# Kernel optimization log

Measured on AMD Instinct MI355X. Metric: run time of the kernel, lower is better.

Reference implementation:

```python
import jax, jax.numpy as jnp
import numpy as np

HIDDEN = 2048
N_HEADS = 16
N_KV_HEADS = 4
HEAD_DIM = HIDDEN // N_HEADS  # 128
BATCH = 1
SEQ = 2048
EPS = 1e-6


def _rms_norm(x, scale, eps=EPS):
    var = jnp.mean(jnp.square(x), axis=-1, keepdims=True)
    return x * jax.lax.rsqrt(var + eps) * scale


def _rotate_half(x):
    x1, x2 = jnp.split(x, 2, axis=-1)
    return jnp.concatenate((-x2, x1), axis=-1)


def setup_inputs() -> dict:
    key = jax.random.key(0)
    ks = jax.random.split(key, 8)
    hidden_states = jax.random.normal(ks[0], (BATCH, SEQ, HIDDEN), dtype=jnp.float32)
    # causal mask, broadcastable over [B, H, S, S]
    attention_mask = jnp.tril(jnp.ones((SEQ, SEQ), dtype=bool))[None, None, :, :]
    # standard RoPE tables, broadcastable against [B, S, H, D]
    inv_freq = 1.0 / (10000.0 ** (np.arange(0, HEAD_DIM, 2, dtype=np.float32) / HEAD_DIM))
    t = np.arange(SEQ, dtype=np.float32)
    freqs = np.outer(t, inv_freq)                      # [S, D/2]
    emb = np.concatenate([freqs, freqs], axis=-1)      # [S, D]
    cos = jnp.asarray(np.cos(emb))[:, None, :]         # [S, 1, D]
    sin = jnp.asarray(np.sin(emb))[:, None, :]
    s = 1.0 / np.sqrt(HIDDEN)
    Wq = jax.random.normal(ks[1], (HIDDEN, N_HEADS * HEAD_DIM), dtype=jnp.float32) * s
    Wk = jax.random.normal(ks[2], (HIDDEN, N_KV_HEADS * HEAD_DIM), dtype=jnp.float32) * s
    Wv = jax.random.normal(ks[3], (HIDDEN, N_KV_HEADS * HEAD_DIM), dtype=jnp.float32) * s
    Wo = jax.random.normal(ks[4], (HIDDEN, HIDDEN), dtype=jnp.float32) * s
    q_norm_scale = jnp.ones((HEAD_DIM,), dtype=jnp.float32)
    k_norm_scale = jnp.ones((HEAD_DIM,), dtype=jnp.float32)
    last_norm_scale = jnp.ones((HIDDEN,), dtype=jnp.float32)
    return {
        "hidden_states": hidden_states,
        "cos": cos,
        "sin": sin,
        "Wq": Wq,
        "Wk": Wk,
        "Wv": Wv,
        "Wo": Wo,
        "q_norm_scale": q_norm_scale,
        "k_norm_scale": k_norm_scale,
        "last_norm_scale": last_norm_scale,
        "attention_mask": attention_mask,
    }


def reference(hidden_states, cos, sin, Wq, Wk, Wv, Wo,
              q_norm_scale, k_norm_scale, last_norm_scale, attention_mask):
    B, S, _ = hidden_states.shape
    q = (hidden_states @ Wq).reshape(B, S, N_HEADS, HEAD_DIM)
    k = (hidden_states @ Wk).reshape(B, S, N_KV_HEADS, HEAD_DIM)
    v = (hidden_states @ Wv).reshape(B, S, N_KV_HEADS, HEAD_DIM)
    # per-head RMSNorm on Q/K
    q = _rms_norm(q, q_norm_scale)
    k = _rms_norm(k, k_norm_scale)
    # RoPE (cos/sin broadcast [S,1,D] -> [B,S,H,D])
    q = q * cos + _rotate_half(q) * sin
    k = k * cos + _rotate_half(k) * sin
    # GQA expansion
    groups = N_HEADS // N_KV_HEADS
    if groups > 1:
        k = jnp.repeat(k, groups, axis=2)
        v = jnp.repeat(v, groups, axis=2)
    out = jax.nn.dot_product_attention(q, k, v, mask=attention_mask)  # [B,S,H,D]
    out = out.reshape(B, S, HIDDEN) @ Wo
    return _rms_norm(out, last_norm_scale)
```

## Files before the change

### kernel.cpp

```cpp
#include <hip/hip_runtime.h>

typedef unsigned short u16;
typedef unsigned int u32;

#define S 2048
#define HID 2048
#define NH 16
#define NKV 4
#define D 128
#define QKVP 3072
#define QSCALE (0.08838834764831845f * 1.4426950408889634f)
#define NEG_INF -3.0e38f

typedef __attribute__((ext_vector_type(8))) short short8;
typedef __attribute__((ext_vector_type(4))) float f32x4;

__device__ __forceinline__ float bf2f(u16 u) {
  union { u32 i; float f; } c; c.i = ((u32)u) << 16; return c.f;
}
__device__ __forceinline__ u16 f2bf(float f) {
  union { float f; u32 i; } c; c.f = f;
  u32 x = c.i;
  u32 r = x + 0x7fffu + ((x >> 16) & 1u);
  return (u16)(r >> 16);
}

#if __has_builtin(__builtin_amdgcn_exp2f)
__device__ __forceinline__ float exp2_hw(float x) { return __builtin_amdgcn_exp2f(x); }
#else
__device__ __forceinline__ float exp2_hw(float x) { return exp2f(x); }
#endif

__device__ __forceinline__ u32 cvt_pk_bf16(float a, float b) {
  u32 r;
  asm("v_cvt_pk_bf16_f32 %0, %1, %2" : "=v"(r) : "v"(a), "v"(b));
  return r;
}

__device__ __forceinline__ void gload16(const u16* g, u16* l) {
  __builtin_amdgcn_global_load_lds(
      (const __attribute__((address_space(1))) u32*)g,
      (__attribute__((address_space(3))) u32*)l, 16, 0, 0);
}

__device__ __forceinline__ void transpose_body(const float* __restrict__ src,
                                               u16* __restrict__ dst,
                                               int N, int K, int nt, int kt,
                                               int t) {
  __shared__ float T[64][65];
#pragma unroll
  for (int it = 0; it < 4; ++it) {
    int r = it * 16 + (t >> 4), c = (t & 15) * 4;
    float4 v = *(const float4*)(src + (size_t)(kt + r) * N + nt + c);
    T[r][c] = v.x; T[r][c + 1] = v.y; T[r][c + 2] = v.z; T[r][c + 3] = v.w;
  }
  __syncthreads();
#pragma unroll
  for (int it = 0; it < 2; ++it) {
    int n = it * 32 + (t >> 3), k8 = (t & 7) * 8;
    ushort4 w0, w1;
    w0.x = f2bf(T[k8 + 0][n]); w0.y = f2bf(T[k8 + 1][n]);
    w0.z = f2bf(T[k8 + 2][n]); w0.w = f2bf(T[k8 + 3][n]);
    w1.x = f2bf(T[k8 + 4][n]); w1.y = f2bf(T[k8 + 5][n]);
    w1.z = f2bf(T[k8 + 6][n]); w1.w = f2bf(T[k8 + 7][n]);
    *(ushort4*)(dst + (size_t)(nt + n) * K + kt + k8) = w0;
    *(ushort4*)(dst + (size_t)(nt + n) * K + kt + k8 + 4) = w1;
  }
}

__global__ __launch_bounds__(256) void k_pre(const float* __restrict__ hidden,
                                             u16* __restrict__ Hb,
                                             const float* __restrict__ Wq,
                                             const float* __restrict__ Wk,
                                             const float* __restrict__ Wv,
                                             u16* __restrict__ WT) {
  const int bx = blockIdx.x, t = threadIdx.x;
  if (bx < 2048) {
    int i = (bx * 256 + t) * 8;
    float4 v0 = *(const float4*)(hidden + i);
    float4 v1 = *(const float4*)(hidden + i + 4);
    ushort4 w0, w1;
    w0.x = f2bf(v0.x); w0.y = f2bf(v0.y); w0.z = f2bf(v0.z); w0.w = f2bf(v0.w);
    w1.x = f2bf(v1.x); w1.y = f2bf(v1.y); w1.z = f2bf(v1.z); w1.w = f2bf(v1.w);
    *(ushort4*)(Hb + i) = w0;
    *(ushort4*)(Hb + i + 4) = w1;
    return;
  }
  const int id = bx - 2048;
  const int x = id % 48, y = id / 48;
  const float* src; u16* dst; int N, nt;
  if (x < 32)      { src = Wq; dst = WT;                    N = 2048; nt = x * 64; }
  else if (x < 40) { src = Wk; dst = WT + 2048ull * 2048;   N = 512;  nt = (x - 32) * 64; }
  else             { src = Wv; dst = WT + 2560ull * 2048;   N = 512;  nt = (x - 40) * 64; }
  transpose_body(src, dst, N, 2048, nt, y * 64, t);
}

__global__ __launch_bounds__(256) void k_transpose(const float* __restrict__ src,
                                                   u16* __restrict__ dst,
                                                   int N, int K) {
  transpose_body(src, dst, N, K, blockIdx.x * 64, blockIdx.y * 64, threadIdx.x);
}

__global__ __launch_bounds__(256) void k_vt(const u16* __restrict__ QKV,
                                            u16* __restrict__ Vt) {
  __shared__ u16 T[64][66];
  const int t = threadIdx.x;
  const int s0 = blockIdx.x * 64, d0 = blockIdx.y * 64;
#pragma unroll
  for (int it = 0; it < 4; ++it) {
    int r = it * 16 + (t >> 4), c = (t & 15) * 4;
    ushort4 v = *(const ushort4*)(QKV + (size_t)(s0 + r) * QKVP + 2560 + d0 + c);
    T[r][c] = v.x; T[r][c + 1] = v.y; T[r][c + 2] = v.z; T[r][c + 3] = v.w;
  }
  __syncthreads();
#pragma unroll
  for (int it = 0; it < 4; ++it) {
    int dd = it * 16 + (t >> 4), sc = (t & 15) * 4;
    ushort4 w;
    w.x = T[sc + 0][dd]; w.y = T[sc + 1][dd];
    w.z = T[sc + 2][dd]; w.w = T[sc + 3][dd];
    *(ushort4*)(Vt + (size_t)(d0 + dd) * S + s0 + sc) = w;
  }
}

__global__ __launch_bounds__(256) void k_gemm_mfma(const u16* __restrict__ A,
                                                   const u16* __restrict__ BT,
                                                   void* __restrict__ Cout,
                                                   int N, int K, int out_bf16) {
  __shared__ __align__(16) u16 As[2][64 * 64];
  __shared__ __align__(16) u16 Bs[2][128 * 64];
  const int t = threadIdx.x, w = t >> 6, lane = t & 63;
  const int l15 = lane & 15, quad = lane >> 4;
  const int m0 = blockIdx.y * 64, n0 = blockIdx.x * 128;

  const int srow = lane >> 3;
  const int schunk = (lane & 7) ^ srow;
  const u16* Agb = A + (size_t)(m0 + w * 8 + srow) * K + schunk * 8;
  const u16* Bgb = BT + (size_t)(n0 + w * 8 + srow) * K + schunk * 8;

  f32x4 acc[4][2];
#pragma unroll
  for (int i = 0; i < 4; ++i)
#pragma unroll
    for (int j = 0; j < 2; ++j) acc[i][j] = (f32x4){0.f, 0.f, 0.f, 0.f};

  auto STAGE = [&](int k0, int b) {
#pragma unroll
    for (int it = 0; it < 2; ++it)
      gload16(Agb + (size_t)it * 32 * K + k0, &As[b][(w * 8 + it * 32) * 64]);
#pragma unroll
    for (int it = 0; it < 4; ++it)
      gload16(Bgb + (size_t)it * 32 * K + k0, &Bs[b][(w * 8 + it * 32) * 64]);
  };

  STAGE(0, 0);
  __syncthreads();
  int cur = 0;
  for (int k0 = 0; k0 < K; k0 += 64) {
    if (k0 + 64 < K) STAGE(k0 + 64, cur ^ 1);

    short8 af[4][2], bf[2][2];
#pragma unroll
    for (int k2 = 0; k2 < 2; ++k2) {
      int ch = (k2 * 4 + quad) ^ (l15 & 7);
#pragma unroll
      for (int i = 0; i < 4; ++i)
        af[i][k2] = *(const short8*)&As[cur][(i * 16 + l15) * 64 + ch * 8];
#pragma unroll
      for (int j = 0; j < 2; ++j)
        bf[j][k2] = *(const short8*)&Bs[cur][(w * 32 + j * 16 + l15) * 64 + ch * 8];
    }
#pragma unroll
    for (int k2 = 0; k2 < 2; ++k2)
#pragma unroll
      for (int i = 0; i < 4; ++i)
#pragma unroll
        for (int j = 0; j < 2; ++j)
          acc[i][j] = __builtin_amdgcn_mfma_f32_16x16x32_bf16(af[i][k2], bf[j][k2], acc[i][j], 0, 0, 0);

    __syncthreads();
    cur ^= 1;
  }

  if (out_bf16) {
    u16* C = (u16*)Cout;
#pragma unroll
    for (int i = 0; i < 4; ++i)
#pragma unroll
      for (int j = 0; j < 2; ++j) {
        int col = n0 + w * 32 + j * 16 + l15;
#pragma unroll
        for (int r = 0; r < 4; ++r)
          C[(size_t)(m0 + i * 16 + quad * 4 + r) * N + col] = f2bf(acc[i][j][r]);
      }
  } else {
    float* C = (float*)Cout;
#pragma unroll
    for (int i = 0; i < 4; ++i)
#pragma unroll
      for (int j = 0; j < 2; ++j) {
        int col = n0 + w * 32 + j * 16 + l15;
#pragma unroll
        for (int r = 0; r < 4; ++r)
          C[(size_t)(m0 + i * 16 + quad * 4 + r) * N + col] = acc[i][j][r];
      }
  }
}

__global__ __launch_bounds__(256) void k_norm_rope(u16* __restrict__ QKV,
                                                   const float* __restrict__ qsc,
                                                   const float* __restrict__ ksc,
                                                   const float* __restrict__ cosp,
                                                   const float* __restrict__ sinp) {
  const int s = blockIdx.x;
  const int w = threadIdx.x >> 6, lane = threadIdx.x & 63;
  const int hh = blockIdx.y * 4 + w;
  u16* row; const float* sc; float scale;
  if (hh < NH) { row = QKV + (size_t)s * QKVP + hh * D;               sc = qsc; scale = QSCALE; }
  else         { row = QKV + (size_t)s * QKVP + 2048 + (hh - NH) * D; sc = ksc; scale = 1.0f; }
  const int d0 = lane * 2;
  u32 pr = *(const u32*)(row + d0);
  float x0 = bf2f((u16)(pr & 0xffffu)), x1 = bf2f((u16)(pr >> 16));
  float v = x0 * x0 + x1 * x1;
#pragma unroll
  for (int o = 32; o; o >>= 1) v += __shfl_xor(v, o, 64);
  float rinv = rsqrtf(v * (1.0f / 128.0f) + 1e-6f) * scale;
  float xn0 = x0 * rinv * sc[d0], xn1 = x1 * rinv * sc[d0 + 1];
  float p0 = __shfl_xor(xn0, 32, 64);
  float p1 = __shfl_xor(xn1, 32, 64);
  float sgn = (lane < 32) ? -1.f : 1.f;
  float2 c  = *(const float2*)(cosp + (size_t)s * D + d0);
  float2 sn = *(const float2*)(sinp + (size_t)s * D + d0);
  float o0 = xn0 * c.x + sgn * p0 * sn.x;
  float o1 = xn1 * c.y + sgn * p1 * sn.y;
  *(u32*)(row + d0) = cvt_pk_bf16(o0, o1);
}

#define KP 128
#define PTP 72

__global__ __launch_bounds__(256) void k_flash(const u16* __restrict__ QKV,
                                               const u16* __restrict__ Vt,
                                               u16* __restrict__ O) {
  const int h = blockIdx.y, g = h >> 2;
  const int qt = (h < 8) ? (31 - (int)blockIdx.x) : (int)blockIdx.x;
  const int t = threadIdx.x;
  const int w = t >> 6, lane = t & 63, l15 = lane & 15, quad = lane >> 4;

  __shared__ __align__(16) u16 Klds[2][64 * KP];
  __shared__ __align__(16) u16 Vlds[128 * 64];
  __shared__ __align__(16) u16 Pt[4][16 * PTP];

  const int qbase = qt * 64 + w * 16;
  const int qrow = qbase + l15;

  short8 qf[4];
  {
    const u16* qp = QKV + (size_t)qrow * QKVP + h * D + quad * 8;
#pragma unroll
    for (int c = 0; c < 4; ++c) qf[c] = *(const short8*)(qp + c * 32);
  }

  float m = NEG_INF, l = 0.f;
  f32x4 oacc[8];
#pragma unroll
  for (int nc = 0; nc < 8; ++nc) oacc[nc] = (f32x4){0.f, 0.f, 0.f, 0.f};

  const int nt = qt + 1;
  const int dd = t >> 3, cc = t & 7;

  auto KLOAD = [&](int j0, int b) {
#pragma unroll
    for (int it = 0; it < 4; ++it) {
      int rl = w * 16 + it * 4 + quad;
      int gchunk = (lane & 15) ^ (rl & 7);
      const u16* gp = QKV + (size_t)(j0 + rl) * QKVP + 2048 + g * D + gchunk * 8;
      gload16(gp, &Klds[b][(w * 16 + it * 4) * KP]);
    }
  };
  auto VLOAD = [&](int j0, uint4* vr) {
#pragma unroll
    for (int it = 0; it < 4; ++it)
      vr[it] = *(const uint4*)(Vt + (size_t)(g * D + dd + it * 32) * S + j0 + cc * 8);
  };
  auto VWRITE = [&](uint4* vr) {
#pragma unroll
    for (int it = 0; it < 4; ++it) {
      int d = dd + it * 32;
      *(uint4*)&Vlds[d * 64 + ((cc ^ (d & 7)) * 8)] = vr[it];
    }
  };
  auto QKT = [&](int b, f32x4* sa) {
#pragma unroll
    for (int sub = 0; sub < 4; ++sub) {
      f32x4 acc = {0.f, 0.f, 0.f, 0.f};
#pragma unroll
      for (int c = 0; c < 4; ++c) {
        int ch = (c * 4 + quad) ^ (l15 & 7);
        short8 kf = *(const short8*)&Klds[b][(sub * 16 + l15) * KP + ch * 8];
        acc = __builtin_amdgcn_mfma_f32_16x16x32_bf16(kf, qf[c], acc, 0, 0, 0);
      }
      sa[sub] = acc;
    }
  };
  auto SMPV = [&](int jt, f32x4* sa) {
    const int j0 = jt * 64;
    if (jt == nt - 1) {
#pragma unroll
      for (int sub = 0; sub < 4; ++sub) {
        int keyb = j0 + sub * 16 + quad * 4;
#pragma unroll
        for (int r = 0; r < 4; ++r)
          if (keyb + r > qrow) sa[sub][r] = NEG_INF;
      }
    }
    float tmax = sa[0][0];
#pragma unroll
    for (int sub = 0; sub < 4; ++sub)
#pragma unroll
      for (int r = 0; r < 4; ++r) tmax = fmaxf(tmax, sa[sub][r]);
    tmax = fmaxf(tmax, __shfl_xor(tmax, 16, 64));
    tmax = fmaxf(tmax, __shfl_xor(tmax, 32, 64));
    float mn = fmaxf(m, tmax);
    float alpha = exp2_hw(m - mn);
    m = mn;
    float rs = 0.f;
#pragma unroll
    for (int sub = 0; sub < 4; ++sub) {
      float p0 = exp2_hw(sa[sub][0] - m);
      float p1 = exp2_hw(sa[sub][1] - m);
      float p2 = exp2_hw(sa[sub][2] - m);
      float p3 = exp2_hw(sa[sub][3] - m);
      rs += (p0 + p1) + (p2 + p3);
      u32 lo = cvt_pk_bf16(p0, p1);
      u32 hi = cvt_pk_bf16(p2, p3);
      *(uint2*)&Pt[w][l15 * PTP + sub * 16 + quad * 4] = make_uint2(lo, hi);
    }
    rs += __shfl_xor(rs, 16, 64);
    rs += __shfl_xor(rs, 32, 64);
    l = l * alpha + rs;
#pragma unroll
    for (int nc = 0; nc < 8; ++nc) {
      oacc[nc][0] *= alpha; oacc[nc][1] *= alpha;
      oacc[nc][2] *= alpha; oacc[nc][3] *= alpha;
    }
#pragma unroll
    for (int kc = 0; kc < 2; ++kc) {
      short8 pf = *(const short8*)&Pt[w][l15 * PTP + kc * 32 + quad * 8];
#pragma unroll
      for (int nc = 0; nc < 8; ++nc) {
        int d = nc * 16 + l15;
        short8 vf = *(const short8*)&Vlds[d * 64 + (((kc * 4 + quad) ^ (d & 7)) * 8)];
        oacc[nc] = __builtin_amdgcn_mfma_f32_16x16x32_bf16(vf, pf, oacc[nc], 0, 0, 0);
      }
    }
  };

  uint4 vrA[4], vrB[4];
  f32x4 sa[4];
  KLOAD(0, 0);
  VLOAD(0, vrA);
  for (int jt = 0; jt < nt; jt += 2) {
    __syncthreads();
    VWRITE(vrA);
    __syncthreads();
    QKT(0, sa);
    if (jt + 1 < nt) { KLOAD((jt + 1) * 64, 1); VLOAD((jt + 1) * 64, vrB); }
    SMPV(jt, sa);
    if (jt + 1 < nt) {
      __syncthreads();
      VWRITE(vrB);
      __syncthreads();
      QKT(1, sa);
      if (jt + 2 < nt) { KLOAD((jt + 2) * 64, 0); VLOAD((jt + 2) * 64, vrA); }
      SMPV(jt + 1, sa);
    }
  }

  float inv = 1.0f / l;
  u16* orow = O + (size_t)qrow * HID + h * D;
#pragma unroll
  for (int nc = 0; nc < 8; ++nc) {
    ushort4 wv;
    wv.x = f2bf(oacc[nc][0] * inv); wv.y = f2bf(oacc[nc][1] * inv);
    wv.z = f2bf(oacc[nc][2] * inv); wv.w = f2bf(oacc[nc][3] * inv);
    *(ushort4*)(orow + nc * 16 + quad * 4) = wv;
  }
}

__device__ __forceinline__ float blockSum256(float v, float* red, int t) {
#pragma unroll
  for (int o = 32; o; o >>= 1) v += __shfl_xor(v, o, 64);
  if ((t & 63) == 0) red[t >> 6] = v;
  __syncthreads();
  v = red[0] + red[1] + red[2] + red[3];
  __syncthreads();
  return v;
}

__global__ __launch_bounds__(256) void k_fnorm(const float* __restrict__ X,
                                               const float* __restrict__ sc,
                                               float* __restrict__ out) {
  const int s = blockIdx.x, t = threadIdx.x;
  const float* row = X + (size_t)s * HID;
  float4 r0 = *(const float4*)(row + t * 8);
  float4 r1 = *(const float4*)(row + t * 8 + 4);
  float x[8] = {r0.x, r0.y, r0.z, r0.w, r1.x, r1.y, r1.z, r1.w};
  float ss = 0.f;
#pragma unroll
  for (int ii = 0; ii < 8; ++ii) ss += x[ii] * x[ii];
  __shared__ float red[4];
  float tot = blockSum256(ss, red, t);
  float rinv = rsqrtf(tot * (1.0f / 2048.0f) + 1e-6f);
  float4 s0 = *(const float4*)(sc + t * 8);
  float4 s1 = *(const float4*)(sc + t * 8 + 4);
  float4 w0 = make_float4(x[0] * rinv * s0.x, x[1] * rinv * s0.y,
                          x[2] * rinv * s0.z, x[3] * rinv * s0.w);
  float4 w1 = make_float4(x[4] * rinv * s1.x, x[5] * rinv * s1.y,
                          x[6] * rinv * s1.z, x[7] * rinv * s1.w);
  *(float4*)(out + (size_t)s * HID + t * 8) = w0;
  *(float4*)(out + (size_t)s * HID + t * 8 + 4) = w1;
}

extern "C" void kernel_launch(void* const* d_in, const int* in_sizes, int n_in,
                              void* d_out, int out_size, void* d_ws, size_t ws_size,
                              hipStream_t stream) {
  const float* hidden = (const float*)d_in[0];
  const float* cosp   = (const float*)d_in[1];
  const float* sinp   = (const float*)d_in[2];
  const float* Wq     = (const float*)d_in[3];
  const float* Wk     = (const float*)d_in[4];
  const float* Wv     = (const float*)d_in[5];
  const float* Wo     = (const float*)d_in[6];
  const float* qsc    = (const float*)d_in[7];
  const float* ksc    = (const float*)d_in[8];
  const float* lsc    = (const float*)d_in[9];
  float* out = (float*)d_out;

  char* ws = (char*)d_ws;
  u16*   Hb  = (u16*)(ws);
  u16*   WoT = (u16*)(ws);
  u16*   WT  = (u16*)(ws + (8ull << 20));
  u16*   An  = (u16*)(ws + (8ull << 20));
  u16*   QKV = (u16*)(ws + (20ull << 20));
  float* Ob  = (float*)(ws + (20ull << 20));
  u16*   Vtb = (u16*)(ws + (32ull << 20));

  k_pre<<<2048 + 1536, 256, 0, stream>>>(hidden, Hb, Wq, Wk, Wv, WT);
  k_gemm_mfma<<<dim3(24, 32), 256, 0, stream>>>(Hb, WT, QKV, QKVP, 2048, 1);
  k_transpose<<<dim3(32, 32), 256, 0, stream>>>(Wo, WoT, 2048, 2048);
  k_norm_rope<<<dim3(S, 5), 256, 0, stream>>>(QKV, qsc, ksc, cosp, sinp);
  k_vt<<<dim3(32, 8), 256, 0, stream>>>(QKV, Vtb);
  k_flash<<<dim3(32, NH), 256, 0, stream>>>(QKV, Vtb, An);
  k_gemm_mfma<<<dim3(16, 32), 256, 0, stream>>>(An, WoT, Ob, 2048, 2048, 0);
  k_fnorm<<<S, 256, 0, stream>>>(Ob, lsc, out);
}
```

Baseline: 285.4 us.

## Fuse QK RMSNorm, RoPE and V transpose into the QKV GEMM epilogue

Replaces the generic QKV GEMM with a specialised kernel whose epilogue applies per-head RMSNorm and RoPE to Q/K tiles, using a shared-memory reduction across waves, and writes V directly transposed into Vt. This removes the separate norm_rope and vt kernels along with their launches and extra global read/write passes over QKV. The prefetch of the next K-slab is also moved after the LDS fragment reads in both GEMMs so loads overlap the MFMA work. The trade-off is extra LDS traffic and two barriers in the epilogue, plus scattered 2-byte stores for Q/K output.

```diff
diff --git a/kernel.cpp b/kernel.cpp
--- a/kernel.cpp
+++ b/kernel.cpp
@@ -101,25 +101,146 @@
   transpose_body(src, dst, N, K, blockIdx.x * 64, blockIdx.y * 64, threadIdx.x);
 }
 
-__global__ __launch_bounds__(256) void k_vt(const u16* __restrict__ QKV,
-                                            u16* __restrict__ Vt) {
-  __shared__ u16 T[64][66];
-  const int t = threadIdx.x;
-  const int s0 = blockIdx.x * 64, d0 = blockIdx.y * 64;
-#pragma unroll
-  for (int it = 0; it < 4; ++it) {
-    int r = it * 16 + (t >> 4), c = (t & 15) * 4;
-    ushort4 v = *(const ushort4*)(QKV + (size_t)(s0 + r) * QKVP + 2560 + d0 + c);
-    T[r][c] = v.x; T[r][c + 1] = v.y; T[r][c + 2] = v.z; T[r][c + 3] = v.w;
-  }
+__global__ __launch_bounds__(256) void k_gemm_qkv(const u16* __restrict__ A,
+                                                  const u16* __restrict__ BT,
+                                                  u16* __restrict__ QKV,
+                                                  u16* __restrict__ Vt,
+                                                  const float* __restrict__ qsc,
+                                                  const float* __restrict__ ksc,
+                                                  const float* __restrict__ cosp,
+                                                  const float* __restrict__ sinp) {
+  __shared__ __align__(16) char smem[49152];
+  u16* AsB = (u16*)smem;
+  u16* BsB = (u16*)(smem + 16384);
+  const int K = 2048;
+  const int t = threadIdx.x, w = t >> 6, lane = t & 63;
+  const int l15 = lane & 15, quad = lane >> 4;
+  const int m0 = blockIdx.y * 64, n0 = blockIdx.x * 128;
+
+  const int srow = lane >> 3;
+  const int schunk = (lane & 7) ^ srow;
+  const u16* Agb = A + (size_t)(m0 + w * 8 + srow) * K + schunk * 8;
+  const u16* Bgb = BT + (size_t)(n0 + w * 8 + srow) * K + schunk * 8;
+
+  f32x4 acc[4][2];
+#pragma unroll
+  for (int i = 0; i < 4; ++i)
+#pragma unroll
+    for (int j = 0; j < 2; ++j) acc[i][j] = (f32x4){0.f, 0.f, 0.f, 0.f};
+
+  auto STAGE = [&](int k0, int b) {
+#pragma unroll
+    for (int it = 0; it < 2; ++it)
+      gload16(Agb + (size_t)it * 32 * K + k0, AsB + b * 4096 + (w * 8 + it * 32) * 64);
+#pragma unroll
+    for (int it = 0; it < 4; ++it)
+      gload16(Bgb + (size_t)it * 32 * K + k0, BsB + b * 8192 + (w * 8 + it * 32) * 64);
+  };
+
+  STAGE(0, 0);
   __syncthreads();
-#pragma unroll
-  for (int it = 0; it < 4; ++it) {
-    int dd = it * 16 + (t >> 4), sc = (t & 15) * 4;
-    ushort4 w;
-    w.x = T[sc + 0][dd]; w.y = T[sc + 1][dd];
-    w.z = T[sc + 2][dd]; w.w = T[sc + 3][dd];
-    *(ushort4*)(Vt + (size_t)(d0 + dd) * S + s0 + sc) = w;
+  int cur = 0;
+  for (int k0 = 0; k0 < K; k0 += 64) {
+    short8 af[4][2], bf[2][2];
+#pragma unroll
+    for (int k2 = 0; k2 < 2; ++k2) {
+      int ch = (k2 * 4 + quad) ^ (l15 & 7);
+#pragma unroll
+      for (int i = 0; i < 4; ++i)
+        af[i][k2] = *(const short8*)&AsB[cur * 4096 + (i * 16 + l15) * 64 + ch * 8];
+#pragma unroll
+      for (int j = 0; j < 2; ++j)
+        bf[j][k2] = *(const short8*)&BsB[cur * 8192 + (w * 32 + j * 16 + l15) * 64 + ch * 8];
+    }
+
+    if (k0 + 64 < K) STAGE(k0 + 64, cur ^ 1);
+
+#pragma unroll
+    for (int k2 = 0; k2 < 2; ++k2)
+#pragma unroll
+      for (int i = 0; i < 4; ++i)
+#pragma unroll
+        for (int j = 0; j < 2; ++j)
+          acc[i][j] = __builtin_amdgcn_mfma_f32_16x16x32_bf16(af[i][k2], bf[j][k2], acc[i][j], 0, 0, 0);
+
+    __syncthreads();
+    cur ^= 1;
+  }
+
+  const int colL0 = w * 32 + l15;
+  const int colL1 = w * 32 + 16 + l15;
+
+  if (n0 < 2560) {
+    const float* sc = (n0 < 2048) ? qsc : ksc;
+    const float scale = (n0 < 2048) ? QSCALE : 1.0f;
+
+    float ssp[4][4];
+#pragma unroll
+    for (int i = 0; i < 4; ++i)
+#pragma unroll
+      for (int r = 0; r < 4; ++r)
+        ssp[i][r] = acc[i][0][r] * acc[i][0][r] + acc[i][1][r] * acc[i][1][r];
+#pragma unroll
+    for (int o = 1; o < 16; o <<= 1)
+#pragma unroll
+      for (int i = 0; i < 4; ++i)
+#pragma unroll
+        for (int r = 0; r < 4; ++r) ssp[i][r] += __shfl_xor(ssp[i][r], o, 64);
+    float* red = (float*)smem;
+    float* X = (float*)(smem + 2048);
+    if (l15 == 0) {
+#pragma unroll
+      for (int i = 0; i < 4; ++i)
+#pragma unroll
+        for (int r = 0; r < 4; ++r) red[w * 64 + i * 16 + quad * 4 + r] = ssp[i][r];
+    }
+    __syncthreads();
+    float rinv[4][4];
+#pragma unroll
+    for (int i = 0; i < 4; ++i)
+#pragma unroll
+      for (int r = 0; r < 4; ++r) {
+        int row = i * 16 + quad * 4 + r;
+        float s = red[row] + red[64 + row] + red[128 + row] + red[192 + row];
+        rinv[i][r] = rsqrtf(s * (1.0f / 128.0f) + 1e-6f) * scale;
+      }
+    float sc0 = sc[colL0], sc1 = sc[colL1];
+#pragma unroll
+    for (int i = 0; i < 4; ++i)
+#pragma unroll
+      for (int r = 0; r < 4; ++r) {
+        int row = i * 16 + quad * 4 + r;
+        X[row * 132 + colL0] = acc[i][0][r] * rinv[i][r] * sc0;
+        X[row * 132 + colL1] = acc[i][1][r] * rinv[i][r] * sc1;
+      }
+    __syncthreads();
+    float sgn0 = (colL0 < 64) ? -1.f : 1.f;
+    float sgn1 = (colL1 < 64) ? -1.f : 1.f;
+#pragma unroll
+    for (int i = 0; i < 4; ++i)
+#pragma unroll
+      for (int r = 0; r < 4; ++r) {
+        int row = i * 16 + quad * 4 + r;
+        int srw = m0 + row;
+        float xn0 = X[row * 132 + colL0], p0 = X[row * 132 + (colL0 ^ 64)];
+        float xn1 = X[row * 132 + colL1], p1 = X[row * 132 + (colL1 ^ 64)];
+        float v0 = xn0 * cosp[srw * D + colL0] + sgn0 * p0 * sinp[srw * D + colL0];
+        float v1 = xn1 * cosp[srw * D + colL1] + sgn1 * p1 * sinp[srw * D + colL1];
+        QKV[(size_t)srw * QKVP + n0 + colL0] = f2bf(v0);
+        QKV[(size_t)srw * QKVP + n0 + colL1] = f2bf(v1);
+      }
+  } else {
+#pragma unroll
+    for (int i = 0; i < 4; ++i) {
+      int sbase = m0 + i * 16 + quad * 4;
+      ushort4 w0, w1;
+      w0.x = f2bf(acc[i][0][0]); w0.y = f2bf(acc[i][0][1]);
+      w0.z = f2bf(acc[i][0][2]); w0.w = f2bf(acc[i][0][3]);
+      w1.x = f2bf(acc[i][1][0]); w1.y = f2bf(acc[i][1][1]);
+      w1.z = f2bf(acc[i][1][2]); w1.w = f2bf(acc[i][1][3]);
+      *(ushort4*)(Vt + (size_t)(n0 - 2560 + colL0) * S + sbase) = w0;
+      *(ushort4*)(Vt + (size_t)(n0 - 2560 + colL1) * S + sbase) = w1;
+    }
   }
 }
 
@@ -157,8 +278,6 @@
   __syncthreads();
   int cur = 0;
   for (int k0 = 0; k0 < K; k0 += 64) {
-    if (k0 + 64 < K) STAGE(k0 + 64, cur ^ 1);
-
     short8 af[4][2], bf[2][2];
 #pragma unroll
     for (int k2 = 0; k2 < 2; ++k2) {
@@ -170,6 +289,9 @@
       for (int j = 0; j < 2; ++j)
         bf[j][k2] = *(const short8*)&Bs[cur][(w * 32 + j * 16 + l15) * 64 + ch * 8];
     }
+
+    if (k0 + 64 < K) STAGE(k0 + 64, cur ^ 1);
+
 #pragma unroll
     for (int k2 = 0; k2 < 2; ++k2)
 #pragma unroll
@@ -205,35 +327,6 @@
           C[(size_t)(m0 + i * 16 + quad * 4 + r) * N + col] = acc[i][j][r];
       }
   }
-}
-
-__global__ __launch_bounds__(256) void k_norm_rope(u16* __restrict__ QKV,
-                                                   const float* __restrict__ qsc,
-                                                   const float* __restrict__ ksc,
-                                                   const float* __restrict__ cosp,
-                                                   const float* __restrict__ sinp) {
-  const int s = blockIdx.x;
-  const int w = threadIdx.x >> 6, lane = threadIdx.x & 63;
-  const int hh = blockIdx.y * 4 + w;
-  u16* row; const float* sc; float scale;
-  if (hh < NH) { row = QKV + (size_t)s * QKVP + hh * D;               sc = qsc; scale = QSCALE; }
-  else         { row = QKV + (size_t)s * QKVP + 2048 + (hh - NH) * D; sc = ksc; scale = 1.0f; }
-  const int d0 = lane * 2;
-  u32 pr = *(const u32*)(row + d0);
-  float x0 = bf2f((u16)(pr & 0xffffu)), x1 = bf2f((u16)(pr >> 16));
-  float v = x0 * x0 + x1 * x1;
-#pragma unroll
-  for (int o = 32; o; o >>= 1) v += __shfl_xor(v, o, 64);
-  float rinv = rsqrtf(v * (1.0f / 128.0f) + 1e-6f) * scale;
-  float xn0 = x0 * rinv * sc[d0], xn1 = x1 * rinv * sc[d0 + 1];
-  float p0 = __shfl_xor(xn0, 32, 64);
-  float p1 = __shfl_xor(xn1, 32, 64);
-  float sgn = (lane < 32) ? -1.f : 1.f;
-  float2 c  = *(const float2*)(cosp + (size_t)s * D + d0);
-  float2 sn = *(const float2*)(sinp + (size_t)s * D + d0);
-  float o0 = xn0 * c.x + sgn * p0 * sn.x;
-  float o1 = xn1 * c.y + sgn * p1 * sn.y;
-  *(u32*)(row + d0) = cvt_pk_bf16(o0, o1);
 }
 
 #define KP 128
@@ -447,10 +540,8 @@
   u16*   Vtb = (u16*)(ws + (32ull << 20));
 
   k_pre<<<2048 + 1536, 256, 0, stream>>>(hidden, Hb, Wq, Wk, Wv, WT);
-  k_gemm_mfma<<<dim3(24, 32), 256, 0, stream>>>(Hb, WT, QKV, QKVP, 2048, 1);
+  k_gemm_qkv<<<dim3(24, 32), 256, 0, stream>>>(Hb, WT, QKV, Vtb, qsc, ksc, cosp, sinp);
   k_transpose<<<dim3(32, 32), 256, 0, stream>>>(Wo, WoT, 2048, 2048);
-  k_norm_rope<<<dim3(S, 5), 256, 0, stream>>>(QKV, qsc, ksc, cosp, sinp);
-  k_vt<<<dim3(32, 8), 256, 0, stream>>>(QKV, Vtb);
   k_flash<<<dim3(32, NH), 256, 0, stream>>>(QKV, Vtb, An);
   k_gemm_mfma<<<dim3(16, 32), 256, 0, stream>>>(An, WoT, Ob, 2048, 2048, 0);
   k_fnorm<<<S, 256, 0, stream>>>(Ob, lsc, out);
```

After: 287.2 us. No clear change (+0.6%).
